# Performance work log

Hardware: AMD Instinct MI355X
Metric: run time of the kernel (lower is better)

The kernel has to match this reference:

```python
import jax, jax.numpy as jnp
import numpy as np

B, N, E = 2, 20000, 200000
IN_F, OUT_F, HEADS = 256, 32, 4
NEG_SLOPE = 0.2


def setup_inputs() -> dict:
    key = jax.random.key(0)
    k1, k2, k3, k4 = jax.random.split(key, 4)
    x = jax.random.normal(k1, (B, N, IN_F), dtype=jnp.float32)
    edge_indices = jax.random.randint(k2, (2, E), 0, N, dtype=jnp.int64)
    # xavier-uniform-like scales
    W = jax.random.normal(k3, (OUT_F * HEADS, IN_F), dtype=jnp.float32) * np.float32(1.0 / np.sqrt(IN_F))
    a = jax.random.normal(k4, (2 * OUT_F, 1), dtype=jnp.float32) * np.float32(0.1)
    return {"x": x, "edge_indices": edge_indices, "W": W, "a": a}


def reference(x, edge_indices, W, a):
    Bq, Nq, _ = x.shape
    Hh, Ff = HEADS, OUT_F
    # h: [B, N, H, F]
    h = (x @ W.T).reshape(Bq, Nq, Hh, Ff)
    src, dst = edge_indices[0], edge_indices[1]
    Eq = src.shape[0]
    h_src = h[:, src]  # [B, E, H, F]
    h_dst = h[:, dst]  # [B, E, H, F]
    # scores = leaky_relu(concat(h_src, h_dst) @ a)  without materializing concat
    a_src, a_dst = a[:Ff, 0], a[Ff:, 0]
    scores = (jnp.einsum('behf,f->beh', h_src, a_src)
              + jnp.einsum('behf,f->beh', h_dst, a_dst))
    scores = jnp.where(scores > 0, scores, NEG_SLOPE * scores)  # LeakyReLU(0.2)
    # Original applies softmax over dim=0 (the BATCH dim) per edge
    sm = jax.nn.softmax(scores, axis=0)  # [B, E, H]
    # Original loop overwrites attention_weights[:, src] per edge, so only the
    # LAST edge with a given src survives.
    edge_ids = jnp.arange(Eq, dtype=jnp.int32)
    last_edge = jax.ops.segment_max(edge_ids, src, num_segments=Nq)
    has_edge = jax.ops.segment_sum(jnp.ones((Eq,), jnp.int32), src, num_segments=Nq) > 0
    last_edge = jnp.clip(last_edge, 0, Eq - 1)
    aw = jnp.where(has_edge[None, :, None], sm[:, last_edge], 0.0)  # [B, N, H]
    # aggregated[:, s] = aw[:, s] * sum_{edges i: src[i]==s} h_dst[:, i]
    seg = jax.ops.segment_sum(jnp.transpose(h_dst, (1, 0, 2, 3)), src, num_segments=Nq)  # [N,B,H,F]
    seg = jnp.transpose(seg, (1, 0, 2, 3))  # [B, N, H, F]
    aggregated = aw[..., None] * seg
    # mean over heads; dropout is identity in eval mode
    return aggregated.mean(axis=2)  # [B, N, F]
```

## Files before the change

### kernel.cpp

```cpp
#include <hip/hip_runtime.h>
#include <hip/hip_bf16.h>

#define BB 2
#define NN 20000
#define EE 200000
#define INF 256
#define OUTF 32
#define NH 4
#define HF 128
#define HF2 256
#define NEG_SLOPE 0.2f
#define GEMM_BLOCKS 625
#define EDGE_BLOCKS 782
#define CAP 48
#define OVF_CAP 8192

using bf16 = __hip_bfloat16;
typedef __attribute__((ext_vector_type(8))) short bf16x8;
typedef __attribute__((ext_vector_type(4))) float f32x4;
typedef unsigned long long u64;

__device__ __forceinline__ float bf2f(unsigned short s){ return __uint_as_float((unsigned)s << 16); }
__device__ __forceinline__ ushort f2bf_bits(float f){
    __hip_bfloat16 b = __float2bfloat16(f);
    return *(ushort*)&b;
}

__device__ __forceinline__ int get_src(const int* ei, int e, int f64){
    return f64 ? ei[2 * e] : ei[e];
}
__device__ __forceinline__ int get_dst(const int* ei, int e, int f64){
    return f64 ? ei[2 * EE + 2 * e] : ei[EE + e];
}

__device__ __forceinline__ size_t hrow_of(int row){
    return (row >= NN) ? ((size_t)(row - NN) * 2 + 1) : ((size_t)row * 2);
}

__global__ void k_init(const ushort* __restrict__ xr, const int* __restrict__ er,
                       const void* __restrict__ Wv,
                       int* __restrict__ flags, ushort* __restrict__ wbf,
                       int* __restrict__ cnt, u64* __restrict__ last_e64,
                       int* __restrict__ ovf_cnt){
    int i = blockIdx.x * blockDim.x + threadIdx.x;
    if (i < NN){ cnt[i] = 0; last_e64[i] = 0ULL; }
    if (i == 0) *ovf_cnt = 0;
    if (blockIdx.x < 16){
        __shared__ int cnt_big, cnt_nz;
        if (threadIdx.x == 0){ cnt_big = 0; cnt_nz = 0; }
        __syncthreads();
        int big = 0;
        for (int k = threadIdx.x; k < 8192; k += blockDim.x){
            unsigned e = ((unsigned)xr[2 * k] >> 7) & 0xff;
            if (e >= 0xC0) big++;
        }
        int nz = 0;
        for (int k = threadIdx.x; k < 4096; k += blockDim.x){
            if (er[2 * k + 1] != 0) nz++;
        }
        atomicAdd(&cnt_big, big);
        atomicAdd(&cnt_nz, nz);
        __syncthreads();
        if (blockIdx.x == 0 && threadIdx.x == 0){
            flags[0] = (cnt_big >= 16) ? 1 : 0;
            flags[1] = (cnt_nz == 0) ? 1 : 0;
        }
        const bool f32w = (cnt_big >= 16);
        int fr = blockIdx.x * 256 + threadIdx.x;
        {
            int lane = fr & 63;
            int t    = (fr >> 6) & 3;
            int kc   = (fr >> 8) & 7;
            int ch   = fr >> 11;
            int col  = ch * 64 + t * 16 + (lane & 15);
            int kb   = kc * 32 + (lane >> 4) * 8;
            bf16x8 v;
            if (f32w){
                const float* wg = (const float*)Wv + (size_t)col * INF + kb;
                #pragma unroll
                for (int j = 0; j < 8; ++j) v[j] = (short)f2bf_bits(wg[j]);
            } else {
                const ushort* wg = (const ushort*)Wv + (size_t)col * INF + kb;
                #pragma unroll
                for (int j = 0; j < 8; ++j) v[j] = (short)wg[j];
            }
            *(bf16x8*)(wbf + (size_t)fr * 8) = v;
        }
    }
}

__global__ __launch_bounds__(256, 2)
void k_gemm(const void* __restrict__ xv_, const ushort* __restrict__ wbf,
            const void* __restrict__ av, const int* __restrict__ ei,
            const int* __restrict__ flags, ushort* __restrict__ h,
            float* __restrict__ alpha_s, float* __restrict__ alpha_d,
            int* __restrict__ cnt, u64* __restrict__ slots,
            u64* __restrict__ last_e64, int* __restrict__ ovf_cnt,
            int* __restrict__ ovf_list){
    if (blockIdx.x < EDGE_BLOCKS){
        int f64 = flags[1];
        int e = blockIdx.x * 256 + threadIdx.x;
        if (e < EE){
            int s = get_src(ei, e, f64);
            int d = get_dst(ei, e, f64);
            u64 pk = ((u64)(unsigned)(e + 1) << 16) | (unsigned)(d & 0xFFFF);
            int idx = atomicAdd(&cnt[s], 1);
            if (idx < CAP) slots[(size_t)s * CAP + idx] = pk;
            else {
                atomicMax(&last_e64[s], pk);
                int o = atomicAdd(ovf_cnt, 1);
                if (o < OVF_CAP) ovf_list[o] = e;
            }
        }
        return;
    }

    const int bid  = blockIdx.x - EDGE_BLOCKS;
    const int tid  = threadIdx.x;
    const int lane = tid & 63;
    const int w    = tid >> 6;
    const int l15  = lane & 15;
    const int q    = lane >> 4;
    const bool f32 = flags[0] != 0;

    const int row0 = bid * 64 + w * 16;

    f32x4 acc[2][4];
    #pragma unroll
    for (int c = 0; c < 2; ++c)
        #pragma unroll
        for (int t = 0; t < 4; ++t) acc[c][t] = (f32x4){0.f, 0.f, 0.f, 0.f};

    if (f32){
        const float* xp = (const float*)xv_ + (size_t)(row0 + l15) * INF + q * 8;
        float4 c0 = ((const float4*)xp)[0];
        float4 c1 = ((const float4*)xp)[1];
        #pragma unroll
        for (int kc = 0; kc < 8; ++kc){
            float4 n0, n1;
            if (kc < 7){
                const float4* p = (const float4*)(xp + (kc + 1) * 32);
                n0 = p[0];
                n1 = p[1];
            }
            bf16x8 afrag;
            afrag[0] = (short)f2bf_bits(c0.x); afrag[1] = (short)f2bf_bits(c0.y);
            afrag[2] = (short)f2bf_bits(c0.z); afrag[3] = (short)f2bf_bits(c0.w);
            afrag[4] = (short)f2bf_bits(c1.x); afrag[5] = (short)f2bf_bits(c1.y);
            afrag[6] = (short)f2bf_bits(c1.z); afrag[7] = (short)f2bf_bits(c1.w);
            #pragma unroll
            for (int c = 0; c < 2; ++c){
                const ushort* wb = wbf + (size_t)c * 16384;
                #pragma unroll
                for (int t = 0; t < 4; ++t){
                    bf16x8 bfrag = *(const bf16x8*)(wb + (((size_t)kc * 4 + t) * 64 + lane) * 8);
                    acc[c][t] = __builtin_amdgcn_mfma_f32_16x16x32_bf16(afrag, bfrag, acc[c][t], 0, 0, 0);
                }
            }
            if (kc < 7){ c0 = n0; c1 = n1; }
        }
    } else {
        const ushort* xp = (const ushort*)xv_ + (size_t)(row0 + l15) * INF + q * 8;
        bf16x8 af = *(const bf16x8*)xp;
        #pragma unroll
        for (int kc = 0; kc < 8; ++kc){
            bf16x8 nf;
            if (kc < 7) nf = *(const bf16x8*)(xp + (kc + 1) * 32);
            #pragma unroll
            for (int c = 0; c < 2; ++c){
                const ushort* wb = wbf + (size_t)c * 16384;
                #pragma unroll
                for (int t = 0; t < 4; ++t){
                    bf16x8 bfrag = *(const bf16x8*)(wb + (((size_t)kc * 4 + t) * 64 + lane) * 8);
                    acc[c][t] = __builtin_amdgcn_mfma_f32_16x16x32_bf16(af, bfrag, acc[c][t], 0, 0, 0);
                }
            }
            if (kc < 7) af = nf;
        }
    }

    #pragma unroll
    for (int r = 0; r < 4; ++r){
        int row = row0 + q * 4 + r;
        ushort* hp_ = h + hrow_of(row) * HF;
        #pragma unroll
        for (int t = 0; t < 2; ++t){
            unsigned v0 = (unsigned)f2bf_bits(acc[0][t][r])
                        | ((unsigned)f2bf_bits(acc[0][t + 2][r]) << 16);
            unsigned v1 = (unsigned)f2bf_bits(acc[1][t][r])
                        | ((unsigned)f2bf_bits(acc[1][t + 2][r]) << 16);
            int f = t * 16 + l15;
            uint2 vv; vv.x = v0; vv.y = v1;
            *(uint2*)(hp_ + f * 4) = vv;
        }
    }

    float as_lo, as_hi, ad_lo, ad_hi;
    if (f32){
        const float* af = (const float*)av;
        as_lo = af[l15];        as_hi = af[16 + l15];
        ad_lo = af[OUTF + l15]; ad_hi = af[OUTF + 16 + l15];
    } else {
        const ushort* ab = (const ushort*)av;
        as_lo = bf2f(ab[l15]);        as_hi = bf2f(ab[16 + l15]);
        ad_lo = bf2f(ab[OUTF + l15]); ad_hi = bf2f(ab[OUTF + 16 + l15]);
    }
    #pragma unroll
    for (int r = 0; r < 4; ++r){
        int row = row0 + q * 4 + r;
        #pragma unroll
        for (int c = 0; c < 2; ++c){
            #pragma unroll
            for (int hp = 0; hp < 2; ++hp){
                int t0 = hp * 2, t1 = hp * 2 + 1;
                float ps = acc[c][t0][r] * as_lo + acc[c][t1][r] * as_hi;
                float pd = acc[c][t0][r] * ad_lo + acc[c][t1][r] * ad_hi;
                ps += __shfl_down(ps, 8, 16); pd += __shfl_down(pd, 8, 16);
                ps += __shfl_down(ps, 4, 16); pd += __shfl_down(pd, 4, 16);
                ps += __shfl_down(ps, 2, 16); pd += __shfl_down(pd, 2, 16);
                ps += __shfl_down(ps, 1, 16); pd += __shfl_down(pd, 1, 16);
                if (l15 == 0){
                    size_t o = (size_t)row * NH + c * 2 + hp;
                    alpha_s[o] = ps;
                    alpha_d[o] = pd;
                }
            }
        }
    }
}

__global__ __launch_bounds__(256)
void k_agg(const u64* __restrict__ slots, const int* __restrict__ cnt,
           const u64* __restrict__ last_e64,
           const float* __restrict__ alpha_s, const float* __restrict__ alpha_d,
           const ushort* __restrict__ h, float* __restrict__ aw,
           float* __restrict__ out_f){
    int lane = threadIdx.x & 63;
    int wid  = (blockIdx.x * blockDim.x + threadIdx.x) >> 6;
    int nw   = (gridDim.x * blockDim.x) >> 6;
    int b = lane >> 5;
    int f = lane & 31;
    int c  = lane & 7;
    int bb = c >> 2;
    int hh = c & 3;
    const ushort* hb = h + b * HF + f * 4;
    for (int n = wid; n < NN; n += nw){
        int m = cnt[n]; if (m > CAP) m = CAP;
        u64 le = last_e64[n];

        const u64* sl = slots + (size_t)n * CAP;
        float ax = 0.f, ay = 0.f, az = 0.f, aww = 0.f;
        int i = 0;
        for (; i + 4 <= m; i += 4){
            ulonglong2 p0 = *(const ulonglong2*)(sl + i);
            ulonglong2 p1 = *(const ulonglong2*)(sl + i + 2);
            le = p0.x > le ? p0.x : le;  le = p0.y > le ? p0.y : le;
            le = p1.x > le ? p1.x : le;  le = p1.y > le ? p1.y : le;
            int d0 = (int)(p0.x & 0xFFFFULL);
            int d1 = (int)(p0.y & 0xFFFFULL);
            int d2 = (int)(p1.x & 0xFFFFULL);
            int d3 = (int)(p1.y & 0xFFFFULL);
            ushort4 u0 = *(const ushort4*)(hb + (size_t)d0 * HF2);
            ushort4 u1 = *(const ushort4*)(hb + (size_t)d1 * HF2);
            ushort4 u2 = *(const ushort4*)(hb + (size_t)d2 * HF2);
            ushort4 u3 = *(const ushort4*)(hb + (size_t)d3 * HF2);
            ax += bf2f(u0.x) + bf2f(u1.x) + bf2f(u2.x) + bf2f(u3.x);
            ay += bf2f(u0.y) + bf2f(u1.y) + bf2f(u2.y) + bf2f(u3.y);
            az += bf2f(u0.z) + bf2f(u1.z) + bf2f(u2.z) + bf2f(u3.z);
            aww += bf2f(u0.w) + bf2f(u1.w) + bf2f(u2.w) + bf2f(u3.w);
        }
        for (; i < m; ++i){
            u64 pk = sl[i];
            le = pk > le ? pk : le;
            int d = (int)(pk & 0xFFFFULL);
            ushort4 u = *(const ushort4*)(hb + (size_t)d * HF2);
            ax += bf2f(u.x); ay += bf2f(u.y); az += bf2f(u.z); aww += bf2f(u.w);
        }

        float my_aw = 0.f;
        if (le != 0ULL){
            int d = (int)(le & 0xFFFFULL);
            float ss = alpha_s[((size_t)bb * NN + n) * NH + hh]
                     + alpha_d[((size_t)bb * NN + d) * NH + hh];
            float so = alpha_s[((size_t)(1 - bb) * NN + n) * NH + hh]
                     + alpha_d[((size_t)(1 - bb) * NN + d) * NH + hh];
            ss = ss > 0.f ? ss : NEG_SLOPE * ss;
            so = so > 0.f ? so : NEG_SLOPE * so;
            float mx = fmaxf(ss, so);
            float e0 = __expf(ss - mx);
            float e1 = __expf(so - mx);
            my_aw = 0.25f * e0 / (e0 + e1);
        }
        if (lane < 8) aw[((size_t)bb * NN + n) * NH + hh] = my_aw;

        float aw0 = __shfl(my_aw, (b << 2) + 0, 8);
        float aw1 = __shfl(my_aw, (b << 2) + 1, 8);
        float aw2 = __shfl(my_aw, (b << 2) + 2, 8);
        float aw3 = __shfl(my_aw, (b << 2) + 3, 8);

        out_f[((size_t)b * NN + n) * OUTF + f] =
            aw0 * ax + aw1 * ay + aw2 * az + aw3 * aww;
    }
}

__global__ void k_fix(const int* __restrict__ ei, const int* __restrict__ flags,
                      const int* __restrict__ ovf_cnt, const int* __restrict__ ovf_list,
                      const ushort* __restrict__ h, const float* __restrict__ aw,
                      float* __restrict__ out_f){
    int lane = threadIdx.x & 63;
    int wid  = (blockIdx.x * blockDim.x + threadIdx.x) >> 6;
    int nw   = (gridDim.x * blockDim.x) >> 6;
    int b = lane >> 5;
    int f = lane & 31;
    int M = *ovf_cnt; if (M > OVF_CAP) M = OVF_CAP;
    int f64 = flags[1];
    for (int i = wid; i < M; i += nw){
        int e = ovf_list[i];
        int s = get_src(ei, e, f64);
        int d = get_dst(ei, e, f64);
        float4 awv = *(const float4*)(aw + ((size_t)b * NN + s) * NH);
        ushort4 u = *(const ushort4*)(h + ((size_t)d * 2 + b) * HF + f * 4);
        float acc = awv.x * bf2f(u.x) + awv.y * bf2f(u.y)
                  + awv.z * bf2f(u.z) + awv.w * bf2f(u.w);
        atomicAdd(&out_f[((size_t)b * NN + s) * OUTF + f], acc);
    }
}

extern "C" void kernel_launch(void* const* d_in, const int* in_sizes, int n_in,
                              void* d_out, int out_size, void* d_ws, size_t ws_size,
                              hipStream_t stream){
    const void* x = d_in[0]; const void* eiv = d_in[1];
    const void* W = d_in[2]; const void* a  = d_in[3];
    for (int i = 0; i < n_in; ++i){
        if      (in_sizes[i] == BB * NN * INF) x   = d_in[i];
        else if (in_sizes[i] == 2 * EE)        eiv = d_in[i];
        else if (in_sizes[i] == HF * INF)      W   = d_in[i];
        else if (in_sizes[i] == 2 * OUTF)      a   = d_in[i];
    }
    const int* ei = (const int*)eiv;
    float* out = (float*)d_out;

    const size_t HN = (size_t)BB * NN * HF;
    char* p = (char*)d_ws;
    int*   flags    = (int*)p;                        p += 64;
    ushort* wbf     = (ushort*)p;                     p += 32768 * 2;
    ushort* h       = (ushort*)p;                     p += HN * 2;
    float* alpha_s  = (float*)p;                      p += (size_t)BB * NN * NH * 4;
    float* alpha_d  = (float*)p;                      p += (size_t)BB * NN * NH * 4;
    float* aw       = (float*)p;                      p += (size_t)BB * NN * NH * 4;
    u64*   last_e64 = (u64*)p;                        p += (size_t)NN * 8;
    int*   cnt      = (int*)p;                        p += (size_t)NN * 4;
    int*   ovf_cnt  = (int*)p;                        p += 64;
    int*   ovf_list = (int*)p;                        p += (size_t)OVF_CAP * 4;
    u64*   slots    = (u64*)p;

    k_init <<<(NN + 255) / 256, 256, 0, stream>>>((const ushort*)x, ei, W, flags, wbf,
                                                  cnt, last_e64, ovf_cnt);
    k_gemm <<<EDGE_BLOCKS + GEMM_BLOCKS, 256, 0, stream>>>(x, wbf, a, ei, flags, h,
                                                           alpha_s, alpha_d, cnt,
                                                           slots, last_e64, ovf_cnt,
                                                           ovf_list);
    k_agg  <<<2048, 256, 0, stream>>>(slots, cnt, last_e64, alpha_s, alpha_d,
                                      h, aw, out);
    k_fix  <<<32, 256, 0, stream>>>(ei, flags, ovf_cnt, ovf_list, h, aw, out);
}
```

Baseline: 144.9 us.

## Split GEMM work across waves by head pair and prefetch all x rows upfront

Each wave now computes a 16-row tile for only one half of the output columns (two heads) instead of all four, halving per-wave accumulators and doubling the GEMM block count. All eight K-chunks of the x row fragment are loaded upfront before the MFMA chain, with a scheduling barrier separating loads from compute. This aims to raise parallelism and memory-level parallelism in the fused GEMM phase. The cost is that each x row fragment is read by two waves instead of one, and h stores become narrower 4-byte writes.

```diff
diff --git a/kernel.cpp b/kernel.cpp
--- a/kernel.cpp
+++ b/kernel.cpp
@@ -10,7 +10,7 @@
 #define HF 128
 #define HF2 256
 #define NEG_SLOPE 0.2f
-#define GEMM_BLOCKS 625
+#define GEMM_BLOCKS 1250
 #define EDGE_BLOCKS 782
 #define CAP 48
 #define OVF_CAP 8192
@@ -123,75 +123,78 @@
     const int q    = lane >> 4;
     const bool f32 = flags[0] != 0;
 
-    const int row0 = bid * 64 + w * 16;
-
-    f32x4 acc[2][4];
+    const int row0 = bid * 32 + (w >> 1) * 16;
+    const int ch   = w & 1;
+    const int hd0  = ch * 2;
+    const ushort* wb = wbf + (size_t)ch * 16384;
+
+    f32x4 acc[4];
     #pragma unroll
-    for (int c = 0; c < 2; ++c)
-        #pragma unroll
-        for (int t = 0; t < 4; ++t) acc[c][t] = (f32x4){0.f, 0.f, 0.f, 0.f};
+    for (int t = 0; t < 4; ++t) acc[t] = (f32x4){0.f, 0.f, 0.f, 0.f};
 
     if (f32){
         const float* xp = (const float*)xv_ + (size_t)(row0 + l15) * INF + q * 8;
-        float4 c0 = ((const float4*)xp)[0];
-        float4 c1 = ((const float4*)xp)[1];
-        #pragma unroll
-        for (int kc = 0; kc < 8; ++kc){
-            float4 n0, n1;
-            if (kc < 7){
-                const float4* p = (const float4*)(xp + (kc + 1) * 32);
-                n0 = p[0];
-                n1 = p[1];
-            }
-            bf16x8 afrag;
-            afrag[0] = (short)f2bf_bits(c0.x); afrag[1] = (short)f2bf_bits(c0.y);
-            afrag[2] = (short)f2bf_bits(c0.z); afrag[3] = (short)f2bf_bits(c0.w);
-            afrag[4] = (short)f2bf_bits(c1.x); afrag[5] = (short)f2bf_bits(c1.y);
-            afrag[6] = (short)f2bf_bits(c1.z); afrag[7] = (short)f2bf_bits(c1.w);
-            #pragma unroll
-            for (int c = 0; c < 2; ++c){
-                const ushort* wb = wbf + (size_t)c * 16384;
-                #pragma unroll
-                for (int t = 0; t < 4; ++t){
-                    bf16x8 bfrag = *(const bf16x8*)(wb + (((size_t)kc * 4 + t) * 64 + lane) * 8);
-                    acc[c][t] = __builtin_amdgcn_mfma_f32_16x16x32_bf16(afrag, bfrag, acc[c][t], 0, 0, 0);
-                }
-            }
-            if (kc < 7){ c0 = n0; c1 = n1; }
-        }
+        float4 a0 = ((const float4*)(xp +   0))[0], b0 = ((const float4*)(xp +   0))[1];
+        float4 a1 = ((const float4*)(xp +  32))[0], b1 = ((const float4*)(xp +  32))[1];
+        float4 a2 = ((const float4*)(xp +  64))[0], b2 = ((const float4*)(xp +  64))[1];
+        float4 a3 = ((const float4*)(xp +  96))[0], b3 = ((const float4*)(xp +  96))[1];
+        float4 a4 = ((const float4*)(xp + 128))[0], b4 = ((const float4*)(xp + 128))[1];
+        float4 a5 = ((const float4*)(xp + 160))[0], b5 = ((const float4*)(xp + 160))[1];
+        float4 a6 = ((const float4*)(xp + 192))[0], b6 = ((const float4*)(xp + 192))[1];
+        float4 a7 = ((const float4*)(xp + 224))[0], b7 = ((const float4*)(xp + 224))[1];
+        __builtin_amdgcn_sched_barrier(0);
+
+        #define KSTEP(KC, LO, HI)                                                        \
+        {                                                                                \
+            bf16x8 afrag;                                                                \
+            afrag[0] = (short)f2bf_bits(LO.x); afrag[1] = (short)f2bf_bits(LO.y);        \
+            afrag[2] = (short)f2bf_bits(LO.z); afrag[3] = (short)f2bf_bits(LO.w);        \
+            afrag[4] = (short)f2bf_bits(HI.x); afrag[5] = (short)f2bf_bits(HI.y);        \
+            afrag[6] = (short)f2bf_bits(HI.z); afrag[7] = (short)f2bf_bits(HI.w);        \
+            _Pragma("unroll")                                                            \
+            for (int t = 0; t < 4; ++t){                                                 \
+                bf16x8 bfrag = *(const bf16x8*)(wb + (((size_t)(KC) * 4 + t) * 64 + lane) * 8); \
+                acc[t] = __builtin_amdgcn_mfma_f32_16x16x32_bf16(afrag, bfrag, acc[t], 0, 0, 0); \
+            }                                                                            \
+        }
+        KSTEP(0, a0, b0) KSTEP(1, a1, b1) KSTEP(2, a2, b2) KSTEP(3, a3, b3)
+        KSTEP(4, a4, b4) KSTEP(5, a5, b5) KSTEP(6, a6, b6) KSTEP(7, a7, b7)
+        #undef KSTEP
     } else {
         const ushort* xp = (const ushort*)xv_ + (size_t)(row0 + l15) * INF + q * 8;
-        bf16x8 af = *(const bf16x8*)xp;
-        #pragma unroll
-        for (int kc = 0; kc < 8; ++kc){
-            bf16x8 nf;
-            if (kc < 7) nf = *(const bf16x8*)(xp + (kc + 1) * 32);
-            #pragma unroll
-            for (int c = 0; c < 2; ++c){
-                const ushort* wb = wbf + (size_t)c * 16384;
-                #pragma unroll
-                for (int t = 0; t < 4; ++t){
-                    bf16x8 bfrag = *(const bf16x8*)(wb + (((size_t)kc * 4 + t) * 64 + lane) * 8);
-                    acc[c][t] = __builtin_amdgcn_mfma_f32_16x16x32_bf16(af, bfrag, acc[c][t], 0, 0, 0);
-                }
-            }
-            if (kc < 7) af = nf;
-        }
+        bf16x8 f0 = *(const bf16x8*)(xp +   0);
+        bf16x8 f1 = *(const bf16x8*)(xp +  32);
+        bf16x8 f2 = *(const bf16x8*)(xp +  64);
+        bf16x8 f3 = *(const bf16x8*)(xp +  96);
+        bf16x8 f4 = *(const bf16x8*)(xp + 128);
+        bf16x8 f5 = *(const bf16x8*)(xp + 160);
+        bf16x8 f6 = *(const bf16x8*)(xp + 192);
+        bf16x8 f7 = *(const bf16x8*)(xp + 224);
+        __builtin_amdgcn_sched_barrier(0);
+
+        #define KSTEP(KC, AF)                                                            \
+        {                                                                                \
+            _Pragma("unroll")                                                            \
+            for (int t = 0; t < 4; ++t){                                                 \
+                bf16x8 bfrag = *(const bf16x8*)(wb + (((size_t)(KC) * 4 + t) * 64 + lane) * 8); \
+                acc[t] = __builtin_amdgcn_mfma_f32_16x16x32_bf16(AF, bfrag, acc[t], 0, 0, 0); \
+            }                                                                            \
+        }
+        KSTEP(0, f0) KSTEP(1, f1) KSTEP(2, f2) KSTEP(3, f3)
+        KSTEP(4, f4) KSTEP(5, f5) KSTEP(6, f6) KSTEP(7, f7)
+        #undef KSTEP
     }
 
     #pragma unroll
     for (int r = 0; r < 4; ++r){
         int row = row0 + q * 4 + r;
-        ushort* hp_ = h + hrow_of(row) * HF;
+        ushort* hp_ = h + hrow_of(row) * HF + hd0;
         #pragma unroll
         for (int t = 0; t < 2; ++t){
-            unsigned v0 = (unsigned)f2bf_bits(acc[0][t][r])
-                        | ((unsigned)f2bf_bits(acc[0][t + 2][r]) << 16);
-            unsigned v1 = (unsigned)f2bf_bits(acc[1][t][r])
-                        | ((unsigned)f2bf_bits(acc[1][t + 2][r]) << 16);
+            unsigned v = (unsigned)f2bf_bits(acc[t][r])
+                       | ((unsigned)f2bf_bits(acc[t + 2][r]) << 16);
             int f = t * 16 + l15;
-            uint2 vv; vv.x = v0; vv.y = v1;
-            *(uint2*)(hp_ + f * 4) = vv;
+            *(unsigned*)(hp_ + f * 4) = v;
         }
     }
 
@@ -209,21 +212,18 @@
     for (int r = 0; r < 4; ++r){
         int row = row0 + q * 4 + r;
         #pragma unroll
-        for (int c = 0; c < 2; ++c){
-            #pragma unroll
-            for (int hp = 0; hp < 2; ++hp){
-                int t0 = hp * 2, t1 = hp * 2 + 1;
-                float ps = acc[c][t0][r] * as_lo + acc[c][t1][r] * as_hi;
-                float pd = acc[c][t0][r] * ad_lo + acc[c][t1][r] * ad_hi;
-                ps += __shfl_down(ps, 8, 16); pd += __shfl_down(pd, 8, 16);
-                ps += __shfl_down(ps, 4, 16); pd += __shfl_down(pd, 4, 16);
-                ps += __shfl_down(ps, 2, 16); pd += __shfl_down(pd, 2, 16);
-                ps += __shfl_down(ps, 1, 16); pd += __shfl_down(pd, 1, 16);
-                if (l15 == 0){
-                    size_t o = (size_t)row * NH + c * 2 + hp;
-                    alpha_s[o] = ps;
-                    alpha_d[o] = pd;
-                }
+        for (int hp = 0; hp < 2; ++hp){
+            int t0 = hp * 2, t1 = hp * 2 + 1;
+            float ps = acc[t0][r] * as_lo + acc[t1][r] * as_hi;
+            float pd = acc[t0][r] * ad_lo + acc[t1][r] * ad_hi;
+            ps += __shfl_down(ps, 8, 16); pd += __shfl_down(pd, 8, 16);
+            ps += __shfl_down(ps, 4, 16); pd += __shfl_down(pd, 4, 16);
+            ps += __shfl_down(ps, 2, 16); pd += __shfl_down(pd, 2, 16);
+            ps += __shfl_down(ps, 1, 16); pd += __shfl_down(pd, 1, 16);
+            if (l15 == 0){
+                size_t o = (size_t)row * NH + hd0 + hp;
+                alpha_s[o] = ps;
+                alpha_d[o] = pd;
             }
         }
     }
```

Result: no change. 143.0 us (-1.3%).
